# Performance work log

Measured on AMD Instinct MI355X. Metric: run time of the kernel, lower is better.

The kernel has to match this reference:

```python
import jax, jax.numpy as jnp
import numpy as np

D_MODEL = 1024
NUM_HEADS = 16
D_K = D_MODEL // NUM_HEADS
B, S = 2, 2048


def setup_inputs() -> dict:
    key = jax.random.key(0)
    ks = jax.random.split(key, 11)
    scale = 1.0 / np.sqrt(D_MODEL)
    inp = {
        "Q": jax.random.normal(ks[0], (B, S, D_MODEL), jnp.float32),
        "K": jax.random.normal(ks[1], (B, S, D_MODEL), jnp.float32),
        "V": jax.random.normal(ks[2], (B, S, D_MODEL), jnp.float32),
        "mask": jnp.tril(jnp.ones((S, S), jnp.int32))[None, None, :, :],  # causal [1,1,S,S]
        "Wq": jax.random.normal(ks[3], (D_MODEL, D_MODEL), jnp.float32) * scale,
        "bq": jax.random.normal(ks[4], (D_MODEL,), jnp.float32) * scale,
        "Wk": jax.random.normal(ks[5], (D_MODEL, D_MODEL), jnp.float32) * scale,
        "bk": jax.random.normal(ks[6], (D_MODEL,), jnp.float32) * scale,
        "Wv": jax.random.normal(ks[7], (D_MODEL, D_MODEL), jnp.float32) * scale,
        "bv": jax.random.normal(ks[8], (D_MODEL,), jnp.float32) * scale,
        "Wo": jax.random.normal(ks[9], (D_MODEL, D_MODEL), jnp.float32) * scale,
        "bo": jax.random.normal(ks[10], (D_MODEL,), jnp.float32) * scale,
    }
    return inp


def _split_heads(x):
    b, s, _ = x.shape
    return x.reshape(b, s, NUM_HEADS, D_K).transpose(0, 2, 1, 3)  # [B,H,S,d_k]


def reference(Q, K, V, mask, Wq, bq, Wk, bk, Wv, bv, Wo, bo):
    q = _split_heads(Q @ Wq.T + bq)
    k = _split_heads(K @ Wk.T + bk)
    v = _split_heads(V @ Wv.T + bv)
    scores = jnp.einsum("bhqd,bhkd->bhqk", q, k) / jnp.sqrt(jnp.float32(D_K))
    scores = jnp.where(mask == 0, jnp.float32(-1e9), scores)
    probs = jax.nn.softmax(scores, axis=-1)
    attn = jnp.einsum("bhqk,bhkd->bhqd", probs, v)  # [B,H,S,d_k]
    attn = attn.transpose(0, 2, 1, 3).reshape(Q.shape[0], Q.shape[1], D_MODEL)
    return attn @ Wo.T + bo
```

## Files before the change

### kernel.cpp

```cpp
#include <hip/hip_runtime.h>
#include <hip/hip_bf16.h>

typedef __attribute__((ext_vector_type(8))) short short8;
typedef __attribute__((ext_vector_type(4))) short short4v;
typedef __attribute__((ext_vector_type(4))) float f32x4;

static __device__ __forceinline__ short f2bf(float f) {
    __hip_bfloat16 h = __float2bfloat16(f);
    return __builtin_bit_cast(short, h);
}

static __device__ __forceinline__ float exp2fast(float x) {
    float r;
    asm("v_exp_f32 %0, %1" : "=v"(r) : "v"(x));
    return r;
}

static __device__ __forceinline__ unsigned cvt_pk_bf16(float a, float b) {
    unsigned r;
    asm("v_cvt_pk_bf16_f32 %0, %1, %2" : "=v"(r) : "v"(a), "v"(b));
    return r;
}

#define GLOAD16(g, l) __builtin_amdgcn_global_load_lds( \
    (const __attribute__((address_space(1))) void*)(g), \
    (__attribute__((address_space(3))) void*)(l), 16, 0, 0)

__global__ __launch_bounds__(256) void convert_qkv(
        const float* __restrict__ a, const float* __restrict__ b, const float* __restrict__ c,
        short* __restrict__ oa, short* __restrict__ ob, short* __restrict__ oc, int n4) {
    const float* in = blockIdx.y == 0 ? a : blockIdx.y == 1 ? b : c;
    short* out = blockIdx.y == 0 ? oa : blockIdx.y == 1 ? ob : oc;
    int i = blockIdx.x * blockDim.x + threadIdx.x;
    int stride = gridDim.x * blockDim.x;
    for (; i < n4; i += stride) {
        f32x4 v = reinterpret_cast<const f32x4*>(in)[i];
        short4v o;
        o.x = f2bf(v.x); o.y = f2bf(v.y); o.z = f2bf(v.z); o.w = f2bf(v.w);
        reinterpret_cast<short4v*>(out)[i] = o;
    }
}

__global__ __launch_bounds__(256) void convert_w(
        const float* __restrict__ a, const float* __restrict__ b,
        const float* __restrict__ c, const float* __restrict__ d,
        short* __restrict__ oa, short* __restrict__ ob,
        short* __restrict__ oc, short* __restrict__ od, int n4) {
    const float* in = blockIdx.y == 0 ? a : blockIdx.y == 1 ? b : blockIdx.y == 2 ? c : d;
    short* out = blockIdx.y == 0 ? oa : blockIdx.y == 1 ? ob : blockIdx.y == 2 ? oc : od;
    int i = blockIdx.x * blockDim.x + threadIdx.x;
    int stride = gridDim.x * blockDim.x;
    for (; i < n4; i += stride) {
        f32x4 v = reinterpret_cast<const f32x4*>(in)[i];
        short4v o;
        o.x = f2bf(v.x); o.y = f2bf(v.y); o.z = f2bf(v.z); o.w = f2bf(v.w);
        reinterpret_cast<short4v*>(out)[i] = o;
    }
}

__global__ __launch_bounds__(256, 3) void gemm_qkv(
        const short* __restrict__ Qb, const short* __restrict__ Kb, const short* __restrict__ Vb,
        const short* __restrict__ Wq, const short* __restrict__ Wk, const short* __restrict__ Wv,
        const float* __restrict__ bq, const float* __restrict__ bk, const float* __restrict__ bv,
        short* __restrict__ q_, short* __restrict__ k_, short* __restrict__ vT) {
    __shared__ __align__(16) short aS[128 * 64];
    __shared__ __align__(16) short bS[128 * 64];
    const int tid = threadIdx.x;
    const int lane = tid & 63;
    const int w = tid >> 6;
    const int wr = w >> 1, wc = w & 1;
    const int l15 = lane & 15, lq = lane >> 4;
    const int lr = lane >> 3;
    const int lcs = ((lane & 7) ^ lr) * 8;
    const int y = blockIdx.y;
    const int wg = (blockIdx.x & 7) * 32 + (blockIdx.x >> 3);
    const int bn = wg & 7;
    const int bm = wg >> 3;

    const short* A = y == 0 ? Qb : y == 1 ? Kb : Vb;
    const short* W = y == 0 ? Wq : y == 1 ? Wk : Wv;
    const float* bias = y == 0 ? bq : y == 1 ? bk : bv;
    const short* Ab = A + (size_t)(bm * 128) * 1024;
    const short* Wb = W + (size_t)(bn * 128) * 1024;

    f32x4 acc[4][4] = {};

    for (int t = 0; t < 16; ++t) {
        const int k0 = t * 64;
#pragma unroll
        for (int j = 0; j < 4; ++j) {
            int r0 = w * 32 + j * 8;
            GLOAD16(&Ab[(size_t)(r0 + lr) * 1024 + k0 + lcs], &aS[r0 * 64]);
        }
#pragma unroll
        for (int j = 0; j < 4; ++j) {
            int r0 = w * 32 + j * 8;
            GLOAD16(&Wb[(size_t)(r0 + lr) * 1024 + k0 + lcs], &bS[r0 * 64]);
        }
        asm volatile("s_waitcnt vmcnt(0)" ::: "memory");
        __builtin_amdgcn_s_barrier();
#pragma unroll
        for (int kf = 0; kf < 2; ++kf) {
            const int ck = ((kf * 4 + lq) ^ (l15 & 7)) * 8;
            short8 af[4], bfr[4];
#pragma unroll
            for (int mi = 0; mi < 4; ++mi)
                af[mi] = *reinterpret_cast<const short8*>(
                    &aS[(wr * 64 + mi * 16 + l15) * 64 + ck]);
#pragma unroll
            for (int ni = 0; ni < 4; ++ni)
                bfr[ni] = *reinterpret_cast<const short8*>(
                    &bS[(wc * 64 + ni * 16 + l15) * 64 + ck]);
#pragma unroll
            for (int mi = 0; mi < 4; ++mi)
#pragma unroll
                for (int ni = 0; ni < 4; ++ni)
                    acc[mi][ni] = __builtin_amdgcn_mfma_f32_16x16x32_bf16(
                        af[mi], bfr[ni], acc[mi][ni], 0, 0, 0);
        }
        asm volatile("s_waitcnt lgkmcnt(0)" ::: "memory");
        __builtin_amdgcn_sched_barrier(0);
        __builtin_amdgcn_s_barrier();
    }

    const float QSCALE = 0.125f * 1.44269504f;
#pragma unroll
    for (int mi = 0; mi < 4; ++mi) {
#pragma unroll
        for (int ni = 0; ni < 4; ++ni) {
#pragma unroll
            for (int i = 0; i < 4; ++i) {
                int m = bm * 128 + wr * 64 + mi * 16 + lq * 4 + i;
                int n = bn * 128 + wc * 64 + ni * 16 + l15;
                float v = acc[mi][ni][i] + bias[n];
                int b = m >> 11, s = m & 2047, h = n >> 6, d = n & 63;
                if (y == 0) {
                    q_[((size_t)(b * 16 + h) * 2048 + s) * 64 + d] = f2bf(v * QSCALE);
                } else if (y == 1) {
                    k_[((size_t)(b * 16 + h) * 2048 + s) * 64 + d] = f2bf(v);
                } else {
                    vT[((size_t)(b * 16 + h) * 64 + d) * 2048 + s] = f2bf(v);
                }
            }
        }
    }
}

__device__ __forceinline__ void gemm_kloop(
        const short* __restrict__ Abase, const short* __restrict__ Wbase,
        short* aSb, short* bSb, f32x4 (&acc)[4][2], int w, int lane) {
    const int lr = lane >> 3;
    const int lcs = ((lane & 7) ^ lr) * 8;
    const int l15 = lane & 15, lq = lane >> 4;
    const int wr = w >> 1, wc = w & 1;
    const int cA0 = ((0 + lq) ^ (l15 & 7)) * 8;
    const int cA1 = ((4 + lq) ^ (l15 & 7)) * 8;

#pragma unroll
    for (int j = 0; j < 4; ++j) {
        int r0 = w * 32 + j * 8;
        GLOAD16(&Abase[(size_t)(r0 + lr) * 1024 + lcs], &aSb[r0 * 64]);
    }
#pragma unroll
    for (int j = 0; j < 2; ++j) {
        int r0 = w * 16 + j * 8;
        GLOAD16(&Wbase[(size_t)(r0 + lr) * 1024 + lcs], &bSb[r0 * 64]);
    }

    for (int t = 0; t < 16; ++t) {
        const int cur = t & 1;
        if (t < 15) {
            const int k0 = (t + 1) * 64;
            const int nb = cur ^ 1;
#pragma unroll
            for (int j = 0; j < 4; ++j) {
                int r0 = w * 32 + j * 8;
                GLOAD16(&Abase[(size_t)(r0 + lr) * 1024 + k0 + lcs], &aSb[nb * 8192 + r0 * 64]);
            }
#pragma unroll
            for (int j = 0; j < 2; ++j) {
                int r0 = w * 16 + j * 8;
                GLOAD16(&Wbase[(size_t)(r0 + lr) * 1024 + k0 + lcs], &bSb[nb * 4096 + r0 * 64]);
            }
            asm volatile("s_waitcnt vmcnt(6)" ::: "memory");
        } else {
            asm volatile("s_waitcnt vmcnt(0)" ::: "memory");
        }
        __builtin_amdgcn_s_barrier();
        __builtin_amdgcn_sched_barrier(0);
#pragma unroll
        for (int kf = 0; kf < 2; ++kf) {
            const int ck = kf ? cA1 : cA0;
            short8 af[4], bfr[2];
#pragma unroll
            for (int mi = 0; mi < 4; ++mi)
                af[mi] = *reinterpret_cast<const short8*>(
                    &aSb[cur * 8192 + (wr * 64 + mi * 16 + l15) * 64 + ck]);
#pragma unroll
            for (int ni = 0; ni < 2; ++ni)
                bfr[ni] = *reinterpret_cast<const short8*>(
                    &bSb[cur * 4096 + (wc * 32 + ni * 16 + l15) * 64 + ck]);
#pragma unroll
            for (int mi = 0; mi < 4; ++mi)
#pragma unroll
                for (int ni = 0; ni < 2; ++ni)
                    acc[mi][ni] = __builtin_amdgcn_mfma_f32_16x16x32_bf16(
                        af[mi], bfr[ni], acc[mi][ni], 0, 0, 0);
        }
        asm volatile("s_waitcnt lgkmcnt(0)" ::: "memory");
        __builtin_amdgcn_sched_barrier(0);
        __builtin_amdgcn_s_barrier();
    }
}

__global__ __launch_bounds__(256, 3) void gemm_o(
        const short* __restrict__ A, const short* __restrict__ W,
        const float* __restrict__ bias, float* __restrict__ out) {
    __shared__ __align__(16) short aSb[2 * 128 * 64];
    __shared__ __align__(16) short bSb[2 * 64 * 64];
    const int tid = threadIdx.x;
    const int lane = tid & 63;
    const int w = tid >> 6;
    const int wg = (blockIdx.x & 7) * 64 + (blockIdx.x >> 3);
    const int bn = wg & 15;
    const int bm = wg >> 4;
    const int l15 = lane & 15, lq = lane >> 4;
    const int wr = w >> 1, wc = w & 1;

    f32x4 acc[4][2] = {};
    gemm_kloop(&A[(size_t)(bm * 128) * 1024], &W[(size_t)(bn * 64) * 1024],
               aSb, bSb, acc, w, lane);

#pragma unroll
    for (int mi = 0; mi < 4; ++mi)
#pragma unroll
        for (int ni = 0; ni < 2; ++ni)
#pragma unroll
            for (int i = 0; i < 4; ++i) {
                int m = bm * 128 + wr * 64 + mi * 16 + lq * 4 + i;
                int n = bn * 64 + wc * 32 + ni * 16 + l15;
                out[(size_t)m * 1024 + n] = acc[mi][ni][i] + bias[n];
            }
}

__global__ __launch_bounds__(256, 4) void attn_fwd(
        const short* __restrict__ qh, const short* __restrict__ kh,
        const short* __restrict__ vT, short* __restrict__ attn) {
    __shared__ __align__(16) short kS[64 * 72];
    __shared__ __align__(16) short vS[64 * 72];
    __shared__ __align__(16) int pS[4][16 * 36];
    const int tid = threadIdx.x;
    const int lane = tid & 63;
    const int w = tid >> 6;
    const int l15 = lane & 15, lq = lane >> 4;
    const int bh = blockIdx.x & 31;
    const int qt = 31 - (blockIdx.x >> 5);
    const int b = bh >> 4, h = bh & 15;
    const size_t head = (size_t)bh * 2048 * 64;
    const short* qp = qh + head;
    const short* kp = kh + head;
    const short* vp = vT + head;
    const int qw0 = qt * 64 + w * 16;

    short8 qf_[2];
#pragma unroll
    for (int kf = 0; kf < 2; ++kf)
        qf_[kf] = *reinterpret_cast<const short8*>(
            &qp[(size_t)(qw0 + l15) * 64 + kf * 32 + lq * 8]);

    f32x4 o[4] = {};
    float m_ = -1e30f, l_ = 0.f;

    const int sr = tid >> 3;
    const int sc = (tid & 7) * 8;

    const int nt = qt + 1;
    short8 kra = *reinterpret_cast<const short8*>(&kp[(size_t)sr * 64 + sc]);
    short8 krb = *reinterpret_cast<const short8*>(&kp[(size_t)(sr + 32) * 64 + sc]);
    short8 vra = *reinterpret_cast<const short8*>(&vp[(size_t)sr * 2048 + sc]);
    short8 vrb = *reinterpret_cast<const short8*>(&vp[(size_t)(sr + 32) * 2048 + sc]);
    *reinterpret_cast<short8*>(&kS[sr * 72 + sc]) = kra;
    *reinterpret_cast<short8*>(&kS[(sr + 32) * 72 + sc]) = krb;
    *reinterpret_cast<short8*>(&vS[sr * 72 + sc]) = vra;
    *reinterpret_cast<short8*>(&vS[(sr + 32) * 72 + sc]) = vrb;
    __syncthreads();

    for (int t = 0; t < nt; ++t) {
        if (t + 1 < nt) {
            kra = *reinterpret_cast<const short8*>(
                &kp[(size_t)((t + 1) * 64 + sr) * 64 + sc]);
            krb = *reinterpret_cast<const short8*>(
                &kp[(size_t)((t + 1) * 64 + sr + 32) * 64 + sc]);
            vra = *reinterpret_cast<const short8*>(
                &vp[(size_t)sr * 2048 + (t + 1) * 64 + sc]);
            vrb = *reinterpret_cast<const short8*>(
                &vp[(size_t)(sr + 32) * 2048 + (t + 1) * 64 + sc]);
        }
        f32x4 s[4] = {};
#pragma unroll
        for (int kf = 0; kf < 2; ++kf) {
            short8 kfr[4];
#pragma unroll
            for (int cf = 0; cf < 4; ++cf)
                kfr[cf] = *reinterpret_cast<const short8*>(
                    &kS[(cf * 16 + l15) * 72 + kf * 32 + lq * 8]);
#pragma unroll
            for (int cf = 0; cf < 4; ++cf)
                s[cf] = __builtin_amdgcn_mfma_f32_16x16x32_bf16(
                    kfr[cf], qf_[kf], s[cf], 0, 0, 0);
        }
        if (t == qt) {
            const int q = qw0 + l15;
#pragma unroll
            for (int cf = 0; cf < 4; ++cf)
#pragma unroll
                for (int i = 0; i < 4; ++i)
                    if (t * 64 + cf * 16 + lq * 4 + i > q) s[cf][i] = -1e30f;
        }
        float pmax = fmaxf(fmaxf(fmaxf(s[0][0], s[0][1]), fmaxf(s[0][2], s[0][3])),
                           fmaxf(fmaxf(s[1][0], s[1][1]), fmaxf(s[1][2], s[1][3])));
        pmax = fmaxf(pmax, fmaxf(fmaxf(fmaxf(s[2][0], s[2][1]), fmaxf(s[2][2], s[2][3])),
                                 fmaxf(fmaxf(s[3][0], s[3][1]), fmaxf(s[3][2], s[3][3]))));
        pmax = fmaxf(pmax, __shfl_xor(pmax, 16));
        pmax = fmaxf(pmax, __shfl_xor(pmax, 32));
        if (!__all(pmax - m_ <= 8.0f)) {
            float mnew = fmaxf(m_, pmax);
            float scl = exp2fast(m_ - mnew);
            m_ = mnew;
            l_ *= scl;
            float s0 = __shfl(scl, lq * 4 + 0);
            float s1 = __shfl(scl, lq * 4 + 1);
            float s2 = __shfl(scl, lq * 4 + 2);
            float s3 = __shfl(scl, lq * 4 + 3);
#pragma unroll
            for (int df = 0; df < 4; ++df) {
                o[df][0] *= s0; o[df][1] *= s1; o[df][2] *= s2; o[df][3] *= s3;
            }
        }
        float rsum = 0.f;
#pragma unroll
        for (int cf = 0; cf < 4; ++cf) {
            float p0 = exp2fast(s[cf][0] - m_);
            float p1 = exp2fast(s[cf][1] - m_);
            float p2 = exp2fast(s[cf][2] - m_);
            float p3 = exp2fast(s[cf][3] - m_);
            rsum += (p0 + p1) + (p2 + p3);
            pS[w][l15 * 36 + cf * 8 + lq * 2 + 0] = cvt_pk_bf16(p0, p1);
            pS[w][l15 * 36 + cf * 8 + lq * 2 + 1] = cvt_pk_bf16(p2, p3);
        }
        rsum += __shfl_xor(rsum, 16);
        rsum += __shfl_xor(rsum, 32);
        l_ += rsum;
        asm volatile("s_waitcnt lgkmcnt(0)" ::: "memory");
        __builtin_amdgcn_sched_barrier(0);
#pragma unroll
        for (int kk = 0; kk < 2; ++kk) {
            short8 pa = *reinterpret_cast<const short8*>(
                &pS[w][l15 * 36 + kk * 16 + lq * 4]);
            short8 vb[4];
#pragma unroll
            for (int df = 0; df < 4; ++df)
                vb[df] = *reinterpret_cast<const short8*>(
                    &vS[(df * 16 + l15) * 72 + kk * 32 + lq * 8]);
#pragma unroll
            for (int df = 0; df < 4; ++df)
                o[df] = __builtin_amdgcn_mfma_f32_16x16x32_bf16(
                    pa, vb[df], o[df], 0, 0, 0);
        }
        __syncthreads();
        if (t + 1 < nt) {
            *reinterpret_cast<short8*>(&kS[sr * 72 + sc]) = kra;
            *reinterpret_cast<short8*>(&kS[(sr + 32) * 72 + sc]) = krb;
            *reinterpret_cast<short8*>(&vS[sr * 72 + sc]) = vra;
            *reinterpret_cast<short8*>(&vS[(sr + 32) * 72 + sc]) = vrb;
        }
        __syncthreads();
    }

#pragma unroll
    for (int i = 0; i < 4; ++i) {
        float li = __shfl(l_, lq * 4 + i);
        float rinv = 1.0f / li;
        int sg = qw0 + lq * 4 + i;
        size_t mrow = (size_t)b * 2048 + sg;
#pragma unroll
        for (int df = 0; df < 4; ++df) {
            int col = h * 64 + df * 16 + l15;
            attn[mrow * 1024 + col] = f2bf(o[df][i] * rinv);
        }
    }
}

extern "C" void kernel_launch(void* const* d_in, const int* in_sizes, int n_in,
                              void* d_out, int out_size, void* d_ws, size_t ws_size,
                              hipStream_t stream) {
    const float* Q  = (const float*)d_in[0];
    const float* K  = (const float*)d_in[1];
    const float* V  = (const float*)d_in[2];
    const float* Wq = (const float*)d_in[4];
    const float* bq = (const float*)d_in[5];
    const float* Wk = (const float*)d_in[6];
    const float* bk = (const float*)d_in[7];
    const float* Wv = (const float*)d_in[8];
    const float* bv = (const float*)d_in[9];
    const float* Wo = (const float*)d_in[10];
    const float* bo = (const float*)d_in[11];

    char* ws = (char*)d_ws;
    short* Qb   = (short*)(ws);
    short* Kb   = (short*)(ws + 8388608);
    short* Vb   = (short*)(ws + 16777216);
    short* Wqb  = (short*)(ws + 25165824);
    short* Wkb  = (short*)(ws + 27262976);
    short* Wvb  = (short*)(ws + 29360128);
    short* Wob  = (short*)(ws + 31457280);
    short* q_   = (short*)(ws + 33554432);
    short* k_   = (short*)(ws + 41943040);
    short* vT   = (short*)(ws + 50331648);
    short* attn = Qb;

    dim3 cb(256);
    convert_qkv<<<dim3(1024, 3), cb, 0, stream>>>(Q, K, V, Qb, Kb, Vb, 4194304 / 4);
    convert_w<<<dim3(512, 4), cb, 0, stream>>>(Wq, Wk, Wv, Wo, Wqb, Wkb, Wvb, Wob, 1048576 / 4);

    gemm_qkv<<<dim3(256, 3), cb, 0, stream>>>(Qb, Kb, Vb, Wqb, Wkb, Wvb,
                                              bq, bk, bv, q_, k_, vT);

    attn_fwd<<<dim3(1024), cb, 0, stream>>>(q_, k_, vT, attn);

    gemm_o<<<dim3(512), cb, 0, stream>>>(attn, Wob, bo, (float*)d_out);
}
```

Baseline: 227.9 us.

## Merge conversion kernels, swizzle attention LDS tiles, pass P via shuffles

The two fp32-to-bf16 conversion launches are merged into one seven-way launch, saving a kernel launch. In attention, the padded K/V shared tiles become unpadded XOR-swizzled tiles to avoid bank conflicts and cut LDS use. The probability tile no longer goes through per-wave LDS with an explicit wait; it is redistributed into the MFMA operand layout using cross-lane shuffles. The shuffles add extra VALU/permute work per tile.

After: 222.1 us. 1.03x faster.

```diff
diff --git a/kernel.cpp b/kernel.cpp
--- a/kernel.cpp
+++ b/kernel.cpp
@@ -4,6 +4,7 @@
 typedef __attribute__((ext_vector_type(8))) short short8;
 typedef __attribute__((ext_vector_type(4))) short short4v;
 typedef __attribute__((ext_vector_type(4))) float f32x4;
+typedef __attribute__((ext_vector_type(4))) int i32x4;
 
 static __device__ __forceinline__ short f2bf(float f) {
     __hip_bfloat16 h = __float2bfloat16(f);
@@ -26,34 +27,32 @@
     (const __attribute__((address_space(1))) void*)(g), \
     (__attribute__((address_space(3))) void*)(l), 16, 0, 0)
 
-__global__ __launch_bounds__(256) void convert_qkv(
-        const float* __restrict__ a, const float* __restrict__ b, const float* __restrict__ c,
-        short* __restrict__ oa, short* __restrict__ ob, short* __restrict__ oc, int n4) {
-    const float* in = blockIdx.y == 0 ? a : blockIdx.y == 1 ? b : c;
-    short* out = blockIdx.y == 0 ? oa : blockIdx.y == 1 ? ob : oc;
+__global__ __launch_bounds__(256) void convert_all(
+        const float* __restrict__ q, const float* __restrict__ k, const float* __restrict__ v,
+        const float* __restrict__ wq, const float* __restrict__ wk,
+        const float* __restrict__ wv, const float* __restrict__ wo,
+        short* __restrict__ oq, short* __restrict__ ok, short* __restrict__ ov,
+        short* __restrict__ owq, short* __restrict__ owk,
+        short* __restrict__ owv, short* __restrict__ owo) {
+    const int y = blockIdx.y;
+    const float* in;
+    short* out;
+    int n4;
+    switch (y) {
+        case 0: in = q;  out = oq;  n4 = 1048576; break;
+        case 1: in = k;  out = ok;  n4 = 1048576; break;
+        case 2: in = v;  out = ov;  n4 = 1048576; break;
+        case 3: in = wq; out = owq; n4 = 262144;  break;
+        case 4: in = wk; out = owk; n4 = 262144;  break;
+        case 5: in = wv; out = owv; n4 = 262144;  break;
+        default: in = wo; out = owo; n4 = 262144; break;
+    }
     int i = blockIdx.x * blockDim.x + threadIdx.x;
     int stride = gridDim.x * blockDim.x;
     for (; i < n4; i += stride) {
-        f32x4 v = reinterpret_cast<const f32x4*>(in)[i];
+        f32x4 vv = reinterpret_cast<const f32x4*>(in)[i];
         short4v o;
-        o.x = f2bf(v.x); o.y = f2bf(v.y); o.z = f2bf(v.z); o.w = f2bf(v.w);
-        reinterpret_cast<short4v*>(out)[i] = o;
-    }
-}
-
-__global__ __launch_bounds__(256) void convert_w(
-        const float* __restrict__ a, const float* __restrict__ b,
-        const float* __restrict__ c, const float* __restrict__ d,
-        short* __restrict__ oa, short* __restrict__ ob,
-        short* __restrict__ oc, short* __restrict__ od, int n4) {
-    const float* in = blockIdx.y == 0 ? a : blockIdx.y == 1 ? b : blockIdx.y == 2 ? c : d;
-    short* out = blockIdx.y == 0 ? oa : blockIdx.y == 1 ? ob : blockIdx.y == 2 ? oc : od;
-    int i = blockIdx.x * blockDim.x + threadIdx.x;
-    int stride = gridDim.x * blockDim.x;
-    for (; i < n4; i += stride) {
-        f32x4 v = reinterpret_cast<const f32x4*>(in)[i];
-        short4v o;
-        o.x = f2bf(v.x); o.y = f2bf(v.y); o.z = f2bf(v.z); o.w = f2bf(v.w);
+        o.x = f2bf(vv.x); o.y = f2bf(vv.y); o.z = f2bf(vv.z); o.w = f2bf(vv.w);
         reinterpret_cast<short4v*>(out)[i] = o;
     }
 }
@@ -246,13 +245,13 @@
 __global__ __launch_bounds__(256, 4) void attn_fwd(
         const short* __restrict__ qh, const short* __restrict__ kh,
         const short* __restrict__ vT, short* __restrict__ attn) {
-    __shared__ __align__(16) short kS[64 * 72];
-    __shared__ __align__(16) short vS[64 * 72];
-    __shared__ __align__(16) int pS[4][16 * 36];
+    __shared__ __align__(16) short kS[64 * 64];
+    __shared__ __align__(16) short vS[64 * 64];
     const int tid = threadIdx.x;
     const int lane = tid & 63;
+    const int l15 = lane & 15, lq = lane >> 4;
     const int w = tid >> 6;
-    const int l15 = lane & 15, lq = lane >> 4;
+    const int hi = (lane >> 5) & 1;
     const int bh = blockIdx.x & 31;
     const int qt = 31 - (blockIdx.x >> 5);
     const int b = bh >> 4, h = bh & 15;
@@ -272,29 +271,32 @@
     float m_ = -1e30f, l_ = 0.f;
 
     const int sr = tid >> 3;
-    const int sc = (tid & 7) * 8;
+    const int sc8 = tid & 7;
+    const int scg = sc8 * 8;
+    const int sls = sr * 64 + (sc8 ^ (sr & 7)) * 8;
+    const int sls2 = (sr + 32) * 64 + (sc8 ^ (sr & 7)) * 8;
 
     const int nt = qt + 1;
-    short8 kra = *reinterpret_cast<const short8*>(&kp[(size_t)sr * 64 + sc]);
-    short8 krb = *reinterpret_cast<const short8*>(&kp[(size_t)(sr + 32) * 64 + sc]);
-    short8 vra = *reinterpret_cast<const short8*>(&vp[(size_t)sr * 2048 + sc]);
-    short8 vrb = *reinterpret_cast<const short8*>(&vp[(size_t)(sr + 32) * 2048 + sc]);
-    *reinterpret_cast<short8*>(&kS[sr * 72 + sc]) = kra;
-    *reinterpret_cast<short8*>(&kS[(sr + 32) * 72 + sc]) = krb;
-    *reinterpret_cast<short8*>(&vS[sr * 72 + sc]) = vra;
-    *reinterpret_cast<short8*>(&vS[(sr + 32) * 72 + sc]) = vrb;
+    short8 kra = *reinterpret_cast<const short8*>(&kp[(size_t)sr * 64 + scg]);
+    short8 krb = *reinterpret_cast<const short8*>(&kp[(size_t)(sr + 32) * 64 + scg]);
+    short8 vra = *reinterpret_cast<const short8*>(&vp[(size_t)sr * 2048 + scg]);
+    short8 vrb = *reinterpret_cast<const short8*>(&vp[(size_t)(sr + 32) * 2048 + scg]);
+    *reinterpret_cast<short8*>(&kS[sls]) = kra;
+    *reinterpret_cast<short8*>(&kS[sls2]) = krb;
+    *reinterpret_cast<short8*>(&vS[sls]) = vra;
+    *reinterpret_cast<short8*>(&vS[sls2]) = vrb;
     __syncthreads();
 
     for (int t = 0; t < nt; ++t) {
         if (t + 1 < nt) {
             kra = *reinterpret_cast<const short8*>(
-                &kp[(size_t)((t + 1) * 64 + sr) * 64 + sc]);
+                &kp[(size_t)((t + 1) * 64 + sr) * 64 + scg]);
             krb = *reinterpret_cast<const short8*>(
-                &kp[(size_t)((t + 1) * 64 + sr + 32) * 64 + sc]);
+                &kp[(size_t)((t + 1) * 64 + sr + 32) * 64 + scg]);
             vra = *reinterpret_cast<const short8*>(
-                &vp[(size_t)sr * 2048 + (t + 1) * 64 + sc]);
+                &vp[(size_t)sr * 2048 + (t + 1) * 64 + scg]);
             vrb = *reinterpret_cast<const short8*>(
-                &vp[(size_t)(sr + 32) * 2048 + (t + 1) * 64 + sc]);
+                &vp[(size_t)(sr + 32) * 2048 + (t + 1) * 64 + scg]);
         }
         f32x4 s[4] = {};
 #pragma unroll
@@ -303,7 +305,7 @@
 #pragma unroll
             for (int cf = 0; cf < 4; ++cf)
                 kfr[cf] = *reinterpret_cast<const short8*>(
-                    &kS[(cf * 16 + l15) * 72 + kf * 32 + lq * 8]);
+                    &kS[(cf * 16 + l15) * 64 + ((kf * 4 + lq) ^ (l15 & 7)) * 8]);
 #pragma unroll
             for (int cf = 0; cf < 4; ++cf)
                 s[cf] = __builtin_amdgcn_mfma_f32_16x16x32_bf16(
@@ -338,6 +340,7 @@
             }
         }
         float rsum = 0.f;
+        unsigned P8[8];
 #pragma unroll
         for (int cf = 0; cf < 4; ++cf) {
             float p0 = exp2fast(s[cf][0] - m_);
@@ -345,23 +348,29 @@
             float p2 = exp2fast(s[cf][2] - m_);
             float p3 = exp2fast(s[cf][3] - m_);
             rsum += (p0 + p1) + (p2 + p3);
-            pS[w][l15 * 36 + cf * 8 + lq * 2 + 0] = cvt_pk_bf16(p0, p1);
-            pS[w][l15 * 36 + cf * 8 + lq * 2 + 1] = cvt_pk_bf16(p2, p3);
+            P8[2 * cf]     = cvt_pk_bf16(p0, p1);
+            P8[2 * cf + 1] = cvt_pk_bf16(p2, p3);
         }
         rsum += __shfl_xor(rsum, 16);
         rsum += __shfl_xor(rsum, 32);
         l_ += rsum;
-        asm volatile("s_waitcnt lgkmcnt(0)" ::: "memory");
-        __builtin_amdgcn_sched_barrier(0);
 #pragma unroll
         for (int kk = 0; kk < 2; ++kk) {
-            short8 pa = *reinterpret_cast<const short8*>(
-                &pS[w][l15 * 36 + kk * 16 + lq * 4]);
+            int dw[4];
+#pragma unroll
+            for (int j = 0; j < 4; ++j) {
+                int src = l15 + 16 * (2 * (lq & 1) + (j >> 1));
+                int vlo = __shfl((int)P8[4 * kk + (j & 1)], src);
+                int vhi = __shfl((int)P8[4 * kk + 2 + (j & 1)], src);
+                dw[j] = hi ? vhi : vlo;
+            }
+            i32x4 dwv; dwv.x = dw[0]; dwv.y = dw[1]; dwv.z = dw[2]; dwv.w = dw[3];
+            short8 pa = __builtin_bit_cast(short8, dwv);
             short8 vb[4];
 #pragma unroll
             for (int df = 0; df < 4; ++df)
                 vb[df] = *reinterpret_cast<const short8*>(
-                    &vS[(df * 16 + l15) * 72 + kk * 32 + lq * 8]);
+                    &vS[(df * 16 + l15) * 64 + ((kk * 4 + lq) ^ (l15 & 7)) * 8]);
 #pragma unroll
             for (int df = 0; df < 4; ++df)
                 o[df] = __builtin_amdgcn_mfma_f32_16x16x32_bf16(
@@ -369,10 +378,10 @@
         }
         __syncthreads();
         if (t + 1 < nt) {
-            *reinterpret_cast<short8*>(&kS[sr * 72 + sc]) = kra;
-            *reinterpret_cast<short8*>(&kS[(sr + 32) * 72 + sc]) = krb;
-            *reinterpret_cast<short8*>(&vS[sr * 72 + sc]) = vra;
-            *reinterpret_cast<short8*>(&vS[(sr + 32) * 72 + sc]) = vrb;
+            *reinterpret_cast<short8*>(&kS[sls]) = kra;
+            *reinterpret_cast<short8*>(&kS[sls2]) = krb;
+            *reinterpret_cast<short8*>(&vS[sls]) = vra;
+            *reinterpret_cast<short8*>(&vS[sls2]) = vrb;
         }
         __syncthreads();
     }
@@ -420,8 +429,8 @@
     short* attn = Qb;
 
     dim3 cb(256);
-    convert_qkv<<<dim3(1024, 3), cb, 0, stream>>>(Q, K, V, Qb, Kb, Vb, 4194304 / 4);
-    convert_w<<<dim3(512, 4), cb, 0, stream>>>(Wq, Wk, Wv, Wo, Wqb, Wkb, Wvb, Wob, 1048576 / 4);
+    convert_all<<<dim3(512, 7), cb, 0, stream>>>(Q, K, V, Wq, Wk, Wv, Wo,
+                                                 Qb, Kb, Vb, Wqb, Wkb, Wvb, Wob);
 
     gemm_qkv<<<dim3(256, 3), cb, 0, stream>>>(Qb, Kb, Vb, Wqb, Wkb, Wvb,
                                               bq, bk, bv, q_, k_, vT);
```
